# Performance work log

Measured on AMD Instinct MI355X. Metric: run time of the kernel, lower is better.

Reference implementation:

```python
import jax, jax.numpy as jnp
import numpy as np

B, L, F = 16, 1080, 2
D = 128          # d_model
NC = 64          # num_cnn_channels
DIN = 256        # expand * d_model
N = 16           # d_state
K = 4            # d_conv
R = 8            # dt_rank = ceil(d_model/16)
OUT = 3
NB = 3           # num_mamba_blocks


def setup_inputs() -> dict:
    key = jax.random.key(0)
    ks = jax.random.split(key, 24)
    nrm = lambda k, shape, s=0.05: (jax.random.normal(k, shape) * s).astype(jnp.float32)
    bn = lambda c: jnp.stack([jnp.ones(c), jnp.zeros(c), jnp.zeros(c), jnp.ones(c)]).astype(jnp.float32)
    return {
        'x': jax.random.normal(ks[0], (B, L, F), dtype=jnp.float32),
        'emb_W': nrm(ks[1], (F, D), 0.5), 'emb_b': jnp.zeros(D, jnp.float32),
        'c3_W': nrm(ks[2], (NC, D, 3)), 'c3_b': jnp.zeros(NC, jnp.float32), 'bn3': bn(NC),
        'c5_W': nrm(ks[3], (NC, D, 5)), 'c5_b': jnp.zeros(NC, jnp.float32), 'bn5': bn(NC),
        'c7_W': nrm(ks[4], (NC, D, 7)), 'c7_b': jnp.zeros(NC, jnp.float32), 'bn7': bn(NC),
        'cf_W': nrm(ks[5], (D, 3 * NC, 1)), 'cf_b': jnp.zeros(D, jnp.float32), 'bnf': bn(D),
        'ln_g': jnp.ones((NB, D), jnp.float32), 'ln_b': jnp.zeros((NB, D), jnp.float32),
        'in_W': nrm(ks[6], (NB, 2 * DIN, D)),
        'mconv_W': nrm(ks[7], (NB, DIN, K), 0.2), 'mconv_b': jnp.zeros((NB, DIN), jnp.float32),
        'xproj_W': nrm(ks[8], (NB, R + 2 * N, DIN)),
        'dt_W': nrm(ks[9], (NB, DIN, R), 0.1), 'dt_b': jnp.full((NB, DIN), -1.0, jnp.float32),
        'A_log': jnp.tile(jnp.log(jnp.arange(1.0, N + 1.0, dtype=jnp.float32)), (NB, DIN, 1)),
        'Dp': jnp.ones((NB, DIN), jnp.float32),
        'out_W': nrm(ks[10], (NB, D, DIN)),
        'flin_W': nrm(ks[11], (D, 2 * D)), 'flin_b': jnp.zeros(D, jnp.float32),
        'fc_W': nrm(ks[12], (OUT, D)), 'fc_b': jnp.zeros(OUT, jnp.float32),
    }


def conv1d(x, W, b, pad):
    # x: (B,C,L), W: (O,C,K)
    y = jax.lax.conv_general_dilated(x, W, (1,), [(pad, pad)],
                                     dimension_numbers=('NCH', 'OIH', 'NCH'))
    return y + b[None, :, None]


def bn_relu(x, bn, eps=1e-5):
    g, b, m, v = bn  # each (C,)
    return jax.nn.relu((x - m[None, :, None]) * (g / jnp.sqrt(v + eps))[None, :, None] + b[None, :, None])


def layernorm(x, g, b, eps=1e-5):
    mu = x.mean(-1, keepdims=True)
    var = ((x - mu) ** 2).mean(-1, keepdims=True)
    return (x - mu) / jnp.sqrt(var + eps) * g + b


def pos_encoding(seq_len, d_model):
    pos = jnp.arange(seq_len, dtype=jnp.float32)[:, None]
    div = jnp.exp(jnp.arange(0, d_model, 2, dtype=jnp.float32) * (-np.log(10000.0) / d_model))
    pe = jnp.zeros((seq_len, d_model), jnp.float32)
    pe = pe.at[:, 0::2].set(jnp.sin(pos * div)).at[:, 1::2].set(jnp.cos(pos * div))
    return pe


def selective_scan(u, dt, A, Bm, Cm, Dp):
    # u,dt: (b,l,d); A: (d,n); Bm,Cm: (b,l,n); Dp: (d,)
    dA = jnp.exp(dt[..., None] * A)                    # (b,l,d,n)
    dBu = (dt * u)[..., None] * Bm[:, :, None, :]      # (b,l,d,n)

    def step(h, t):
        dA_t, dBu_t, C_t = t
        h = dA_t * h + dBu_t                           # (b,d,n)
        return h, jnp.einsum('bdn,bn->bd', h, C_t)

    h0 = jnp.zeros((u.shape[0], u.shape[2], A.shape[1]), u.dtype)
    _, ys = jax.lax.scan(step, h0, (jnp.swapaxes(dA, 0, 1), jnp.swapaxes(dBu, 0, 1), jnp.swapaxes(Cm, 0, 1)))
    return jnp.swapaxes(ys, 0, 1) + u * Dp


def mamba_block(x, in_W, conv_W, conv_b, xproj_W, dt_W, dt_b, A_log, Dp, out_W):
    xz = x @ in_W.T                                    # (b,l,2*din)
    xs, z = jnp.split(xz, 2, axis=-1)
    xc = jnp.swapaxes(xs, 1, 2)                        # (b,din,l)
    xc = jax.lax.conv_general_dilated(xc, conv_W[:, None, :], (1,), [(K - 1, 0)],
                                      dimension_numbers=('NCH', 'OIH', 'NCH'),
                                      feature_group_count=DIN)
    u = jax.nn.silu(jnp.swapaxes(xc + conv_b[None, :, None], 1, 2))  # (b,l,din)
    dbl = u @ xproj_W.T
    dt, Bm, Cm = dbl[..., :R], dbl[..., R:R + N], dbl[..., R + N:]
    dt = jax.nn.softplus(dt @ dt_W.T + dt_b)
    A = -jnp.exp(A_log)
    y = selective_scan(u, dt, A, Bm, Cm, Dp)
    return (y * jax.nn.silu(z)) @ out_W.T


def reference(x, emb_W, emb_b, c3_W, c3_b, bn3, c5_W, c5_b, bn5, c7_W, c7_b, bn7,
              cf_W, cf_b, bnf, ln_g, ln_b, in_W, mconv_W, mconv_b, xproj_W,
              dt_W, dt_b, A_log, Dp, out_W, flin_W, flin_b, fc_W, fc_b):
    xe = x @ emb_W + emb_b + pos_encoding(x.shape[1], emb_W.shape[1])  # (B,L,D)
    ci = jnp.swapaxes(xe, 1, 2)                                        # (B,D,L)
    o3 = bn_relu(conv1d(ci, c3_W, c3_b, 1), bn3)
    o5 = bn_relu(conv1d(ci, c5_W, c5_b, 2), bn5)
    o7 = bn_relu(conv1d(ci, c7_W, c7_b, 3), bn7)
    cc = jnp.concatenate([o3, o5, o7], axis=1)                         # (B,3*NC,L)
    cf = bn_relu(conv1d(cc, cf_W, cf_b, 0), bnf)
    cnn_feat = jnp.swapaxes(cf, 1, 2)                                  # (B,L,D)
    m = xe
    for i in range(NB):  # Sequential(LN, Mamba, Dropout) -- no residual, dropout=eval
        m = mamba_block(layernorm(m, ln_g[i], ln_b[i]), in_W[i], mconv_W[i], mconv_b[i],
                        xproj_W[i], dt_W[i], dt_b[i], A_log[i], Dp[i], out_W[i])
    fused = jax.nn.relu(jnp.concatenate([cnn_feat, m], axis=-1) @ flin_W.T + flin_b)
    pooled = fused.mean(axis=1)                                        # AdaptiveAvgPool1d(1)
    return pooled @ fc_W.T + fc_b
```

## Files before the change

### kernel.cpp

```cpp
#include <hip/hip_runtime.h>
#include <math.h>

#define LSEQ   1080
#define NBATCH 16
#define BLROWS (LSEQ*NBATCH)
#define CHN    27
#define LCH    40

typedef __bf16  bf16x8 __attribute__((ext_vector_type(8)));
typedef float   f32x4  __attribute__((ext_vector_type(4)));
typedef short   short8 __attribute__((ext_vector_type(8)));
typedef short   short4v __attribute__((ext_vector_type(4)));

__device__ __forceinline__ float silu_f(float x) { return x / (1.f + __expf(-x)); }

__device__ __forceinline__ unsigned short f2bf(float f) {
    unsigned int u = __float_as_uint(f);
    u += 0x7fffu + ((u >> 16) & 1u);
    return (unsigned short)(u >> 16);
}
__device__ __forceinline__ float bf2f(unsigned short h) {
    return __uint_as_float(((unsigned int)h) << 16);
}
__device__ __forceinline__ void split_bf(float v, unsigned short& h, unsigned short& l) {
    h = f2bf(v);
    l = f2bf(v - bf2f(h));
}

__global__ __launch_bounds__(256) void embed_kernel(
    const float* __restrict__ x, const float* __restrict__ embW,
    const float* __restrict__ embb, float* __restrict__ xe,
    unsigned short* __restrict__ xeh, unsigned short* __restrict__ xel)
{
    int idx = blockIdx.x * 256 + threadIdx.x;
    if (idx >= BLROWS * 128) return;
    int d = idx & 127;
    int r = idx >> 7;
    int t = r % LSEQ;
    float x0 = x[(size_t)r * 2], x1 = x[(size_t)r * 2 + 1];
    int i2 = d & 126;
    float div = expf((float)i2 * (-9.210340371976184f / 128.f));
    float arg = (float)t * div;
    float pe = (d & 1) ? cosf(arg) : sinf(arg);
    float v = fmaf(x0, embW[d], fmaf(x1, embW[128 + d], embb[d] + pe));
    xe[idx] = v;
    unsigned short h, l;
    split_bf(v, h, l);
    xeh[idx] = h; xel[idx] = l;
}

#define JOB_W192  172032
#define JOB_CF    196608
#define JOB_IN    393216
#define JOB_XP    442368
#define JOB_OT    540672
#define JOB_FL    573440
#define JOB_END   574080
__global__ __launch_bounds__(256) void convw_all(
    const float* __restrict__ c3W, const float* __restrict__ c5W,
    const float* __restrict__ c7W, const float* __restrict__ cfW,
    const float* __restrict__ inW, const float* __restrict__ xpW,
    const float* __restrict__ otW, const float* __restrict__ flW,
    const float* __restrict__ c3b, const float* __restrict__ c5b, const float* __restrict__ c7b,
    const float* __restrict__ bn3, const float* __restrict__ bn5, const float* __restrict__ bn7,
    const float* __restrict__ cfb, const float* __restrict__ bnf,
    unsigned short* __restrict__ w192h, unsigned short* __restrict__ w192l,
    unsigned short* __restrict__ cfh, unsigned short* __restrict__ cfl,
    unsigned short* __restrict__ inh, unsigned short* __restrict__ inl,
    unsigned short* __restrict__ xph, unsigned short* __restrict__ xpl,
    unsigned short* __restrict__ oth, unsigned short* __restrict__ otl,
    unsigned short* __restrict__ flh, unsigned short* __restrict__ fll,
    float* __restrict__ schpack)
{
    int idx = blockIdx.x * 256 + threadIdx.x;
    if (idx >= JOB_END) return;
    float v;
    unsigned short *dh, *dl;
    int off;
    if (idx < JOB_W192) {
        off = idx;
        int n = off / 896, kk = off % 896;
        int slot = kk >> 7, d = kk & 127;
        int br = n >> 6, c = n & 63;
        int KT = 3 + 2 * br, pad = 1 + br;
        int tp = slot - 3 + pad;
        const float* w = (br == 0) ? c3W : (br == 1) ? c5W : c7W;
        v = (tp >= 0 && tp < KT) ? w[((c << 7) + d) * KT + tp] : 0.f;
        dh = w192h; dl = w192l;
    } else if (idx < JOB_CF) {
        off = idx - JOB_W192; v = cfW[off]; dh = cfh; dl = cfl;
    } else if (idx < JOB_IN) {
        off = idx - JOB_CF; v = inW[off]; dh = inh; dl = inl;
    } else if (idx < JOB_XP) {
        off = idx - JOB_IN;
        int k = off & 255, n = (off >> 8) & 63, blk = off >> 14;
        v = (n < 40) ? xpW[((size_t)blk * 40 + n) * 256 + k] : 0.f;
        dh = xph; dl = xpl;
    } else if (idx < JOB_OT) {
        off = idx - JOB_XP; v = otW[off]; dh = oth; dl = otl;
    } else if (idx < JOB_FL) {
        off = idx - JOB_OT; v = flW[off]; dh = flh; dl = fll;
    } else {
        int j = idx - JOB_FL;
        if (j < 384) {
            int col = (j < 192) ? j : j - 192;
            int isSh = j >= 192;
            int br = col >> 6, c = col & 63;
            const float* bn = (br == 0) ? bn3 : (br == 1) ? bn5 : bn7;
            float bias = ((br == 0) ? c3b : (br == 1) ? c5b : c7b)[c];
            float g = bn[c], bb = bn[64 + c], m = bn[128 + c], vv = bn[192 + c];
            float scale = g * rsqrtf(vv + 1e-5f);
            float shift = (bias - m) * scale + bb;
            schpack[j] = isSh ? shift : scale;
        } else {
            int j2 = j - 384;
            int col = j2 & 127;
            int isSh = j2 >= 128;
            float g = bnf[col], bb = bnf[128 + col], m = bnf[256 + col], vv = bnf[384 + col];
            float scale = g * rsqrtf(vv + 1e-5f);
            float shift = (cfb[col] - m) * scale + bb;
            schpack[384 + j2] = isSh ? shift : scale;
        }
        return;
    }
    unsigned short h, l;
    split_bf(v, h, l);
    dh[off] = h; dl[off] = l;
}

__global__ __launch_bounds__(256) void gemm_conv(
    const unsigned short* __restrict__ Xh, const unsigned short* __restrict__ Xl,
    const unsigned short* __restrict__ Wh, const unsigned short* __restrict__ Wl,
    const float* __restrict__ sc, const float* __restrict__ sh,
    unsigned short* __restrict__ Ch, unsigned short* __restrict__ Cl)
{
    __shared__ unsigned short Ah[70][40], Al[70][40];
    __shared__ unsigned short Bh[64][136], Bl[64][136];
    const int tid = threadIdx.x;
    const int n0 = blockIdx.x * 64, t0 = blockIdx.y * 64, b = blockIdx.z;
    const size_t boff = (size_t)b * LSEQ;
    const int lane = tid & 63, wid = tid >> 6;
    const int wr = wid >> 1, wc = wid & 1;
    const int fr = lane & 15, fq = lane >> 4;
    const short8 zz = {0, 0, 0, 0, 0, 0, 0, 0};
    f32x4 acc[2][2];
#pragma unroll
    for (int m = 0; m < 2; ++m)
#pragma unroll
        for (int n = 0; n < 2; ++n) acc[m][n] = (f32x4){0.f, 0.f, 0.f, 0.f};

    for (int ks = 0; ks < 128; ks += 32) {
#pragma unroll
        for (int l = 0; l < 2; ++l) {
            int c = tid + l * 256;
            if (c < 280) {
                int row = c >> 2, kc = (c & 3) << 3;
                int ts = t0 - 3 + row;
                short8 vh = zz, vl = zz;
                if (ts >= 0 && ts < LSEQ) {
                    size_t s = (boff + ts) * 128 + ks + kc;
                    vh = *(const short8*)&Xh[s];
                    vl = *(const short8*)&Xl[s];
                }
                *(short8*)&Ah[row][kc] = vh;
                *(short8*)&Al[row][kc] = vl;
            }
        }
        for (int g = 0; g < 2; ++g) {
            const int ntap = (g == 0) ? 4 : 3;
#pragma unroll
            for (int l = 0; l < 4; ++l) {
                int c = tid + l * 256;
                int col = c >> 4, rem = c & 15, tt = rem >> 2, kq = (rem & 3) << 3;
                if (tt < ntap) {
                    int tap = g * 4 + tt;
                    size_t s = (size_t)(n0 + col) * 896 + tap * 128 + ks + kq;
                    *(short8*)&Bh[col][tt * 32 + kq] = *(const short8*)&Wh[s];
                    *(short8*)&Bl[col][tt * 32 + kq] = *(const short8*)&Wl[s];
                }
            }
            __syncthreads();
            for (int tt = 0; tt < ntap; ++tt) {
                int tap = g * 4 + tt;
                bf16x8 bhf[2], blf[2];
#pragma unroll
                for (int n = 0; n < 2; ++n) {
                    int col = wc * 32 + n * 16 + fr;
                    bhf[n] = __builtin_bit_cast(bf16x8, *(const short8*)&Bh[col][tt * 32 + fq * 8]);
                    blf[n] = __builtin_bit_cast(bf16x8, *(const short8*)&Bl[col][tt * 32 + fq * 8]);
                }
#pragma unroll
                for (int m = 0; m < 2; ++m) {
                    int rowA = wr * 32 + m * 16 + fr + tap;
                    bf16x8 ahf = __builtin_bit_cast(bf16x8, *(const short8*)&Ah[rowA][fq * 8]);
                    bf16x8 alf = __builtin_bit_cast(bf16x8, *(const short8*)&Al[rowA][fq * 8]);
#pragma unroll
                    for (int n = 0; n < 2; ++n) {
                        acc[m][n] = __builtin_amdgcn_mfma_f32_16x16x32_bf16(ahf, bhf[n], acc[m][n], 0, 0, 0);
                        acc[m][n] = __builtin_amdgcn_mfma_f32_16x16x32_bf16(ahf, blf[n], acc[m][n], 0, 0, 0);
                        acc[m][n] = __builtin_amdgcn_mfma_f32_16x16x32_bf16(alf, bhf[n], acc[m][n], 0, 0, 0);
                    }
                }
            }
            __syncthreads();
        }
    }
    unsigned short* Chb = Ch + (size_t)b * LSEQ * 192;
    unsigned short* Clb = Cl + (size_t)b * LSEQ * 192;
#pragma unroll
    for (int m = 0; m < 2; ++m) {
#pragma unroll
        for (int n = 0; n < 2; ++n) {
            int colg = n0 + wc * 32 + n * 16 + fr;
            float scl = sc[colg], shf2 = sh[colg];
#pragma unroll
            for (int r = 0; r < 4; ++r) {
                int t = t0 + wr * 32 + m * 16 + fq * 4 + r;
                if (t >= LSEQ) continue;
                float v = fmaf(acc[m][n][r], scl, shf2);
                v = v > 0.f ? v : 0.f;
                unsigned short h, l;
                split_bf(v, h, l);
                Chb[(size_t)t * 192 + colg] = h;
                Clb[(size_t)t * 192 + colg] = l;
            }
        }
    }
}

template<int BM, int BN>
__global__ __launch_bounds__(256) void gemm_plain(
    const unsigned short* __restrict__ Aph, const unsigned short* __restrict__ Apl, int lda,
    const unsigned short* __restrict__ Wh, const unsigned short* __restrict__ Wl, int Kd,
    int Ntot, int epi,
    const float* __restrict__ sc, const float* __restrict__ sh, const float* __restrict__ bias,
    float* __restrict__ Cf, int ldc,
    unsigned short* __restrict__ Ch, unsigned short* __restrict__ Cl, int ldch)
{
    constexpr int WM = BM / 2, WN = BN / 2;
    constexpr int MR = WM / 16, NR = WN / 16;
    constexpr int ACH = (BM * 4) / 256;
    constexpr int BCH = (BN * 4) / 256;
    __shared__ unsigned short Ah[BM][40], Al[BM][40];
    __shared__ unsigned short Bh[BN][40], Bl[BN][40];
    const int tid = threadIdx.x;
    const int b = blockIdx.z, t0 = blockIdx.y * BM, n0 = blockIdx.x * BN;
    const unsigned short* Abh = Aph + (size_t)b * LSEQ * lda;
    const unsigned short* Abl = Apl + (size_t)b * LSEQ * lda;
    const int lane = tid & 63, wid = tid >> 6;
    const int wr = wid >> 1, wc = wid & 1;
    const int fr = lane & 15, fq = lane >> 4;
    f32x4 acc[MR][NR];
#pragma unroll
    for (int m = 0; m < MR; ++m)
#pragma unroll
        for (int n = 0; n < NR; ++n) acc[m][n] = (f32x4){0.f, 0.f, 0.f, 0.f};

    const short8 zz = {0, 0, 0, 0, 0, 0, 0, 0};
    for (int ks = 0; ks < Kd; ks += 32) {
#pragma unroll
        for (int l = 0; l < ACH; ++l) {
            int c = tid + l * 256;
            int row = c >> 2, kc = (c & 3) << 3;
            int t = t0 + row;
            short8 vh = zz, vl = zz;
            if (t < LSEQ) {
                size_t s = (size_t)t * lda + ks + kc;
                vh = *(const short8*)&Abh[s];
                vl = *(const short8*)&Abl[s];
            }
            *(short8*)&Ah[row][kc] = vh;
            *(short8*)&Al[row][kc] = vl;
        }
#pragma unroll
        for (int l = 0; l < BCH; ++l) {
            int c = tid + l * 256;
            int col = c >> 2, kc = (c & 3) << 3;
            size_t s = (size_t)(n0 + col) * Kd + ks + kc;
            *(short8*)&Bh[col][kc] = *(const short8*)&Wh[s];
            *(short8*)&Bl[col][kc] = *(const short8*)&Wl[s];
        }
        __syncthreads();
        bf16x8 bhf[NR], blf[NR];
#pragma unroll
        for (int n = 0; n < NR; ++n) {
            int col = wc * WN + n * 16 + fr;
            bhf[n] = __builtin_bit_cast(bf16x8, *(const short8*)&Bh[col][fq * 8]);
            blf[n] = __builtin_bit_cast(bf16x8, *(const short8*)&Bl[col][fq * 8]);
        }
#pragma unroll
        for (int m = 0; m < MR; ++m) {
            int rowr = wr * WM + m * 16 + fr;
            bf16x8 ahf = __builtin_bit_cast(bf16x8, *(const short8*)&Ah[rowr][fq * 8]);
            bf16x8 alf = __builtin_bit_cast(bf16x8, *(const short8*)&Al[rowr][fq * 8]);
#pragma unroll
            for (int n = 0; n < NR; ++n) {
                acc[m][n] = __builtin_amdgcn_mfma_f32_16x16x32_bf16(ahf, bhf[n], acc[m][n], 0, 0, 0);
                acc[m][n] = __builtin_amdgcn_mfma_f32_16x16x32_bf16(ahf, blf[n], acc[m][n], 0, 0, 0);
                acc[m][n] = __builtin_amdgcn_mfma_f32_16x16x32_bf16(alf, bhf[n], acc[m][n], 0, 0, 0);
            }
        }
        __syncthreads();
    }

    float* Cfb = Cf ? Cf + (size_t)b * LSEQ * ldc : nullptr;
    unsigned short* Chb = Ch ? Ch + (size_t)b * LSEQ * ldch : nullptr;
    unsigned short* Clb = Cl ? Cl + (size_t)b * LSEQ * ldch : nullptr;
#pragma unroll
    for (int m = 0; m < MR; ++m) {
#pragma unroll
        for (int n = 0; n < NR; ++n) {
            int colg = n0 + wc * WN + n * 16 + fr;
            if (colg >= Ntot) continue;
#pragma unroll
            for (int r = 0; r < 4; ++r) {
                int t = t0 + wr * WM + m * 16 + fq * 4 + r;
                if (t >= LSEQ) continue;
                float v = acc[m][n][r];
                if (epi == 0) {
                    Cfb[(size_t)t * ldc + colg] = v;
                } else if (epi == 1) {
                    v = fmaf(v, sc[colg], sh[colg]);
                    v = v > 0.f ? v : 0.f;
                    unsigned short h, l;
                    split_bf(v, h, l);
                    Chb[(size_t)t * ldch + colg] = h;
                    Clb[(size_t)t * ldch + colg] = l;
                } else if (epi == 2) {
                    v += bias[colg];
                    v = v > 0.f ? v : 0.f;
                    Cfb[(size_t)t * ldc + colg] = v;
                } else {
                    unsigned short h, l;
                    split_bf(v, h, l);
                    Chb[(size_t)t * ldch + colg] = h;
                    Clb[(size_t)t * ldch + colg] = l;
                }
            }
        }
    }
}

__global__ __launch_bounds__(256) void ln_kernel(
    const float* __restrict__ in, const float* __restrict__ g,
    const float* __restrict__ b2, unsigned short* __restrict__ oh,
    unsigned short* __restrict__ ol)
{
    int lane = threadIdx.x & 63;
    int wid  = threadIdx.x >> 6;
    int row = blockIdx.x * 4 + wid;
    if (row >= BLROWS) return;
    const float* rp = in + (size_t)row * 128;
    float v0 = rp[lane], v1 = rp[lane + 64];
    float s = v0 + v1;
#pragma unroll
    for (int o2 = 32; o2 > 0; o2 >>= 1) s += __shfl_xor(s, o2, 64);
    float mu = s * (1.f / 128.f);
    float d0 = v0 - mu, d1 = v1 - mu;
    float q = d0 * d0 + d1 * d1;
#pragma unroll
    for (int o2 = 32; o2 > 0; o2 >>= 1) q += __shfl_xor(q, o2, 64);
    float rs = 1.f / sqrtf(q * (1.f / 128.f) + 1e-5f);
    float y0 = d0 * rs * g[lane]      + b2[lane];
    float y1 = d1 * rs * g[lane + 64] + b2[lane + 64];
    unsigned short h, l;
    size_t o = (size_t)row * 128;
    split_bf(y0, h, l); oh[o + lane] = h;      ol[o + lane] = l;
    split_bf(y1, h, l); oh[o + lane + 64] = h; ol[o + lane + 64] = l;
}

__global__ __launch_bounds__(256) void mconv_kernel(
    const float* __restrict__ xz, const float* __restrict__ Wc,
    const float* __restrict__ bc, float* __restrict__ u,
    unsigned short* __restrict__ uh, unsigned short* __restrict__ ul)
{
    int idx = blockIdx.x * 256 + threadIdx.x;
    int c = idx & 255;
    int r = idx >> 8;
    if (r >= BLROWS) return;
    int t = r % LSEQ;
    const float* xs = xz + (size_t)r * 512 + c;
    float acc = bc[c];
    if (t >= 3) acc = fmaf(xs[-3 * 512], Wc[c * 4 + 0], acc);
    if (t >= 2) acc = fmaf(xs[-2 * 512], Wc[c * 4 + 1], acc);
    if (t >= 1) acc = fmaf(xs[-1 * 512], Wc[c * 4 + 2], acc);
    acc = fmaf(xs[0], Wc[c * 4 + 3], acc);
    float uv = silu_f(acc);
    size_t o = (size_t)r * 256 + c;
    u[o] = uv;
    unsigned short h, l;
    split_bf(uv, h, l);
    uh[o] = h; ul[o] = l;
}

__global__ __launch_bounds__(256) void dtk_kernel(
    const float* __restrict__ dbl, const float* __restrict__ dtW,
    const float* __restrict__ dtb, float* __restrict__ dtout)
{
    int idx = blockIdx.x * 256 + threadIdx.x;
    int c = idx & 255;
    int r = idx >> 8;
    if (r >= BLROWS) return;
    const float* dr = dbl + (size_t)r * 40;
    float a = dtb[c];
#pragma unroll
    for (int j = 0; j < 8; ++j) a = fmaf(dr[j], dtW[c * 8 + j], a);
    float sp = (a > 20.f) ? a : log1pf(__expf(a));
    dtout[(size_t)r * 256 + c] = sp;
}

__global__ __launch_bounds__(256) void scan1_kernel(
    const float* __restrict__ dt, const float* __restrict__ u,
    const float* __restrict__ dbl, const float* __restrict__ Alog,
    float* __restrict__ P, float* __restrict__ S)
{
    __shared__ float sdt[40][64], su[40][64], sB[40][16];
    int bid = blockIdx.x;
    int dg = bid & 3;
    int rest = bid >> 2;
    int ch = rest % CHN;
    int b  = rest / CHN;
    int tid = threadIdx.x;
    int ng = tid & 3, di = tid >> 2;
    int d0 = dg * 64, d = d0 + di, n0 = ng * 4;
    int r0 = b * LSEQ + ch * LCH;
#pragma unroll
    for (int l = 0; l < 3; ++l) {
        int j = tid + l * 256;
        if (j < 640) {
            int row = j >> 4, q = (j & 15) << 2;
            size_t s = (size_t)(r0 + row) * 256 + d0 + q;
            *(float4*)&sdt[row][q] = *(const float4*)&dt[s];
            *(float4*)&su [row][q] = *(const float4*)&u [s];
        }
    }
    if (tid < 160) {
        int row = tid >> 2, q = (tid & 3) << 2;
        *(float4*)&sB[row][q] = *(const float4*)&dbl[(size_t)(r0 + row) * 40 + 8 + q];
    }
    float A2[4];
#pragma unroll
    for (int j = 0; j < 4; ++j) A2[j] = -__expf(Alog[d * 16 + n0 + j]);
    float p[4] = {1.f, 1.f, 1.f, 1.f}, s[4] = {0.f, 0.f, 0.f, 0.f};
    __syncthreads();
#pragma unroll 4
    for (int qi = 0; qi < LCH; ++qi) {
        float dtv = sdt[qi][di];
        float dtu = dtv * su[qi][di];
        float4 Br = *(const float4*)&sB[qi][n0];
        float bv[4] = {Br.x, Br.y, Br.z, Br.w};
#pragma unroll
        for (int j = 0; j < 4; ++j) {
            float a = __expf(dtv * A2[j]);
            p[j] *= a;
            s[j] = fmaf(a, s[j], dtu * bv[j]);
        }
    }
    size_t ob = ((size_t)(b * CHN + ch) * 256 + d) * 16 + n0;
    *(float4*)&P[ob] = make_float4(p[0], p[1], p[2], p[3]);
    *(float4*)&S[ob] = make_float4(s[0], s[1], s[2], s[3]);
}

__global__ __launch_bounds__(256) void scan2_kernel(
    const float* __restrict__ P, const float* __restrict__ S, float* __restrict__ H0)
{
    int idx = blockIdx.x * 256 + threadIdx.x;
    int n = idx & 15;
    int d = (idx >> 4) & 255;
    int b = idx >> 12;
    float h = 0.f;
    for (int ch = 0; ch < CHN; ++ch) {
        size_t o = ((size_t)(b * CHN + ch) * 256 + d) * 16 + n;
        H0[o] = h;
        h = fmaf(P[o], h, S[o]);
    }
}

__global__ __launch_bounds__(256) void scan3_kernel(
    const float* __restrict__ dt, const float* __restrict__ u,
    const float* __restrict__ dbl, const float* __restrict__ Alog,
    const float* __restrict__ H0, const float* __restrict__ Dp,
    const float* __restrict__ xz, unsigned short* __restrict__ gh,
    unsigned short* __restrict__ gl)
{
    __shared__ float sdt[40][64], su[40][64], sz[40][64], sB[40][16], sC[40][16];
    int bid = blockIdx.x;
    int dg = bid & 3;
    int rest = bid >> 2;
    int ch = rest % CHN;
    int b  = rest / CHN;
    int tid = threadIdx.x;
    int ng = tid & 3, di = tid >> 2;
    int d0 = dg * 64, d = d0 + di, n0 = ng * 4;
    int r0 = b * LSEQ + ch * LCH;
#pragma unroll
    for (int l = 0; l < 3; ++l) {
        int j = tid + l * 256;
        if (j < 640) {
            int row = j >> 4, q = (j & 15) << 2;
            size_t s = (size_t)(r0 + row) * 256 + d0 + q;
            *(float4*)&sdt[row][q] = *(const float4*)&dt[s];
            *(float4*)&su [row][q] = *(const float4*)&u [s];
            *(float4*)&sz [row][q] = *(const float4*)&xz[(size_t)(r0 + row) * 512 + 256 + d0 + q];
        }
    }
    if (tid < 160) {
        int row = tid >> 2, q = (tid & 3) << 2;
        *(float4*)&sB[row][q] = *(const float4*)&dbl[(size_t)(r0 + row) * 40 + 8 + q];
        *(float4*)&sC[row][q] = *(const float4*)&dbl[(size_t)(r0 + row) * 40 + 24 + q];
    }
    float A2[4];
#pragma unroll
    for (int j = 0; j < 4; ++j) A2[j] = -__expf(Alog[d * 16 + n0 + j]);
    size_t ob = ((size_t)(b * CHN + ch) * 256 + d) * 16 + n0;
    float4 h4 = *(const float4*)&H0[ob];
    float h[4] = {h4.x, h4.y, h4.z, h4.w};
    float Dpd = Dp[d];
    __syncthreads();
    for (int qi = 0; qi < LCH; ++qi) {
        float dtv = sdt[qi][di];
        float uv  = su[qi][di];
        float dtu = dtv * uv;
        float4 Br = *(const float4*)&sB[qi][n0];
        float4 Cr = *(const float4*)&sC[qi][n0];
        float bv[4] = {Br.x, Br.y, Br.z, Br.w};
        float cv[4] = {Cr.x, Cr.y, Cr.z, Cr.w};
        float pacc = 0.f;
#pragma unroll
        for (int j = 0; j < 4; ++j) {
            float a = __expf(dtv * A2[j]);
            h[j] = fmaf(a, h[j], dtu * bv[j]);
            pacc = fmaf(h[j], cv[j], pacc);
        }
        float acc = pacc + __shfl_xor(pacc, 1);
        acc += __shfl_xor(acc, 2);
        float yv = fmaf(uv, Dpd, acc);
        float gv = yv * silu_f(sz[qi][di]);
        if (ng == 0) sz[qi][di] = gv;
    }
    __syncthreads();
#pragma unroll
    for (int l = 0; l < 3; ++l) {
        int j = tid + l * 256;
        if (j < 640) {
            int row = j >> 4, q = (j & 15) << 2;
            float4 gv4 = *(const float4*)&sz[row][q];
            float gv[4] = {gv4.x, gv4.y, gv4.z, gv4.w};
            alignas(8) unsigned short hs[4], ls[4];
#pragma unroll
            for (int jj = 0; jj < 4; ++jj) split_bf(gv[jj], hs[jj], ls[jj]);
            size_t o = (size_t)(r0 + row) * 256 + d0 + q;
            *(short4v*)&gh[o] = *(short4v*)hs;
            *(short4v*)&gl[o] = *(short4v*)ls;
        }
    }
}

__global__ __launch_bounds__(128) void pool1_kernel(
    const float* __restrict__ fused, float* __restrict__ part)
{
    int d = threadIdx.x;
    int blk = blockIdx.x;
    int ch = blk % CHN;
    int b  = blk / CHN;
    int t0 = ch * LCH;
    float s = 0.f;
    for (int q = 0; q < LCH; ++q)
        s += fused[((size_t)(b * LSEQ + t0 + q)) * 128 + d];
    part[(size_t)(b * CHN + ch) * 128 + d] = s;
}

__global__ __launch_bounds__(128) void pool2_kernel(
    const float* __restrict__ part, const float* __restrict__ fcW,
    const float* __restrict__ fcb, float* __restrict__ out)
{
    __shared__ float pl[128];
    int d = threadIdx.x;
    int b = blockIdx.x;
    float s = 0.f;
    for (int ch = 0; ch < CHN; ++ch) s += part[(size_t)(b * CHN + ch) * 128 + d];
    pl[d] = s * (1.f / 1080.f);
    __syncthreads();
    if (d < 3) {
        float a = fcb[d];
        for (int dd = 0; dd < 128; ++dd) a = fmaf(pl[dd], fcW[d * 128 + dd], a);
        out[b * 3 + d] = a;
    }
}

extern "C" void kernel_launch(void* const* d_in, const int* in_sizes, int n_in,
                              void* d_out, int out_size, void* d_ws, size_t ws_size,
                              hipStream_t stream)
{
    const float* x    = (const float*)d_in[0];
    const float* embW = (const float*)d_in[1];
    const float* embb = (const float*)d_in[2];
    const float* c3W  = (const float*)d_in[3];
    const float* c3b  = (const float*)d_in[4];
    const float* bn3  = (const float*)d_in[5];
    const float* c5W  = (const float*)d_in[6];
    const float* c5b  = (const float*)d_in[7];
    const float* bn5  = (const float*)d_in[8];
    const float* c7W  = (const float*)d_in[9];
    const float* c7b  = (const float*)d_in[10];
    const float* bn7  = (const float*)d_in[11];
    const float* cfW  = (const float*)d_in[12];
    const float* cfb  = (const float*)d_in[13];
    const float* bnf  = (const float*)d_in[14];
    const float* lng  = (const float*)d_in[15];
    const float* lnb  = (const float*)d_in[16];
    const float* inW  = (const float*)d_in[17];
    const float* mcW  = (const float*)d_in[18];
    const float* mcb  = (const float*)d_in[19];
    const float* xpW  = (const float*)d_in[20];
    const float* dtW  = (const float*)d_in[21];
    const float* dtbp = (const float*)d_in[22];
    const float* Alog = (const float*)d_in[23];
    const float* Dp   = (const float*)d_in[24];
    const float* outW = (const float*)d_in[25];
    const float* flW  = (const float*)d_in[26];
    const float* flb  = (const float*)d_in[27];
    const float* fcW  = (const float*)d_in[28];
    const float* fcb  = (const float*)d_in[29];

    float* ws = (float*)d_ws;
    size_t off = 0;
    auto alloc = [&](size_t n) { float* p = ws + off; off += n; return p; };
    float* xe   = alloc((size_t)BLROWS * 128);
    float* xz   = alloc((size_t)BLROWS * 512);
    float* ub   = alloc((size_t)BLROWS * 256);
    float* dtt  = alloc((size_t)BLROWS * 256);
    float* dbl  = alloc((size_t)BLROWS * 40);
    float* Pb   = alloc((size_t)NBATCH * CHN * 256 * 16);
    float* Sb   = alloc((size_t)NBATCH * CHN * 256 * 16);
    float* h0b  = alloc((size_t)NBATCH * CHN * 256 * 16);
    float* schpack = alloc(640);
    float* fused = xz;
    float* mtail = xz + (size_t)BLROWS * 384;

    off = (off + 3) & ~(size_t)3;
    unsigned short* us = (unsigned short*)(ws + off);
    size_t uo = 0;
    auto ualloc = [&](size_t n) { unsigned short* p = us + uo; uo += n; return p; };
    unsigned short* cch  = ualloc((size_t)BLROWS * 192);
    unsigned short* ccl  = ualloc((size_t)BLROWS * 192);
    unsigned short* finh = ualloc((size_t)BLROWS * 256);
    unsigned short* finl = ualloc((size_t)BLROWS * 256);
    unsigned short* ubh  = ualloc((size_t)BLROWS * 256);
    unsigned short* ubl  = ualloc((size_t)BLROWS * 256);
    unsigned short* xeh  = ualloc((size_t)BLROWS * 128);
    unsigned short* xel  = ualloc((size_t)BLROWS * 128);
    unsigned short* w192h = ualloc((size_t)192 * 896); unsigned short* w192l = ualloc((size_t)192 * 896);
    unsigned short* cfh = ualloc(128 * 192); unsigned short* cfl = ualloc(128 * 192);
    unsigned short* inh = ualloc((size_t)1536 * 128); unsigned short* inl = ualloc((size_t)1536 * 128);
    unsigned short* xph = ualloc((size_t)3 * 64 * 256); unsigned short* xpl = ualloc((size_t)3 * 64 * 256);
    unsigned short* oth = ualloc((size_t)384 * 256); unsigned short* otl = ualloc((size_t)384 * 256);
    unsigned short* flh = ualloc((size_t)128 * 256); unsigned short* fll = ualloc((size_t)128 * 256);
    unsigned short* lnxh = cch;
    unsigned short* lnxl = ccl;
    unsigned short* gbh  = ubh;
    unsigned short* gbl  = ubl;
    (void)ws_size; (void)in_sizes; (void)n_in; (void)out_size;

    convw_all<<<(JOB_END + 255) / 256, 256, 0, stream>>>(
        c3W, c5W, c7W, cfW, inW, xpW, outW, flW,
        c3b, c5b, c7b, bn3, bn5, bn7, cfb, bnf,
        w192h, w192l, cfh, cfl, inh, inl, xph, xpl, oth, otl, flh, fll, schpack);

    embed_kernel<<<(BLROWS * 128) / 256, 256, 0, stream>>>(x, embW, embb, xe, xeh, xel);

    dim3 gconv(3, 17, NBATCH);
    gemm_conv<<<gconv, 256, 0, stream>>>(xeh, xel, w192h, w192l, schpack, schpack + 192, cch, ccl);
    dim3 g17(1, 17, NBATCH);
    gemm_plain<64, 128><<<g17, 256, 0, stream>>>(
        cch, ccl, 192, cfh, cfl, 192, 128, 1,
        schpack + 384, schpack + 512, nullptr, nullptr, 0, finh, finl, 256);

    const int SCAN_BLKS = NBATCH * CHN * 4;
    for (int i = 0; i < 3; ++i) {
        const float* min_ = (i == 0) ? xe : mtail;

        ln_kernel<<<BLROWS / 4, 256, 0, stream>>>(min_, lng + i * 128, lnb + i * 128, lnxh, lnxl);

        dim3 gin(4, 17, NBATCH);
        gemm_plain<64, 128><<<gin, 256, 0, stream>>>(
            lnxh, lnxl, 128, inh + (size_t)i * 512 * 128, inl + (size_t)i * 512 * 128, 128,
            512, 0, nullptr, nullptr, nullptr, xz, 512, nullptr, nullptr, 0);

        mconv_kernel<<<BLROWS, 256, 0, stream>>>(xz, mcW + i * 256 * 4, mcb + i * 256, ub, ubh, ubl);

        gemm_plain<64, 64><<<g17, 256, 0, stream>>>(
            ubh, ubl, 256, xph + (size_t)i * 64 * 256, xpl + (size_t)i * 64 * 256, 256,
            40, 0, nullptr, nullptr, nullptr, dbl, 40, nullptr, nullptr, 0);

        dtk_kernel<<<BLROWS, 256, 0, stream>>>(dbl, dtW + i * 256 * 8, dtbp + i * 256, dtt);

        scan1_kernel<<<SCAN_BLKS, 256, 0, stream>>>(
            dtt, ub, dbl, Alog + i * 256 * 16, Pb, Sb);
        scan2_kernel<<<(NBATCH * 256 * 16) / 256, 256, 0, stream>>>(Pb, Sb, h0b);
        scan3_kernel<<<SCAN_BLKS, 256, 0, stream>>>(
            dtt, ub, dbl, Alog + i * 256 * 16, h0b, Dp + i * 256, xz, gbh, gbl);

        if (i < 2) {
            gemm_plain<64, 128><<<g17, 256, 0, stream>>>(
                gbh, gbl, 256, oth + (size_t)i * 128 * 256, otl + (size_t)i * 128 * 256, 256,
                128, 0, nullptr, nullptr, nullptr, mtail, 128, nullptr, nullptr, 0);
        } else {
            gemm_plain<64, 128><<<g17, 256, 0, stream>>>(
                gbh, gbl, 256, oth + (size_t)i * 128 * 256, otl + (size_t)i * 128 * 256, 256,
                128, 3, nullptr, nullptr, nullptr, nullptr, 0, finh + 128, finl + 128, 256);
        }
    }

    gemm_plain<64, 128><<<g17, 256, 0, stream>>>(
        finh, finl, 256, flh, fll, 256, 128, 2,
        nullptr, nullptr, flb, fused, 128, nullptr, nullptr, 0);

    pool1_kernel<<<NBATCH * CHN, 128, 0, stream>>>(fused, Pb);
    pool2_kernel<<<NBATCH, 128, 0, stream>>>(Pb, fcW, fcb, (float*)d_out);
}
```

Before: 648.6 us.

## Fold dt projection into x_proj GEMM and fuse LayerNorm into out-proj epilogue

Precomputes a combined weight, dtW·xpW_dt, so that a single GEMM produces both the dt pre-activation (with bias and softplus applied in the epilogue) and the B/C columns. This removes the separate dtk kernel and the intermediate dbl round trip. The out-projection GEMM for blocks 0 and 1 now computes a LayerNorm over the 128 output columns in its epilogue and writes bf16 hi/lo directly, which drops two ln_kernel launches and the fp32 mtail buffer. The trade-offs are a wider x_proj GEMM (288 columns instead of 40) and an extra cross-warp reduction with syncs in the out-proj epilogue.

```diff
diff --git a/kernel.cpp b/kernel.cpp
--- a/kernel.cpp
+++ b/kernel.cpp
@@ -52,22 +52,23 @@
 #define JOB_W192  172032
 #define JOB_CF    196608
 #define JOB_IN    393216
-#define JOB_XP    442368
-#define JOB_OT    540672
-#define JOB_FL    573440
-#define JOB_END   574080
+#define JOB_WX    638976
+#define JOB_OT    737280
+#define JOB_FL    770048
+#define JOB_END   770688
 __global__ __launch_bounds__(256) void convw_all(
     const float* __restrict__ c3W, const float* __restrict__ c5W,
     const float* __restrict__ c7W, const float* __restrict__ cfW,
     const float* __restrict__ inW, const float* __restrict__ xpW,
-    const float* __restrict__ otW, const float* __restrict__ flW,
+    const float* __restrict__ dtW, const float* __restrict__ otW,
+    const float* __restrict__ flW,
     const float* __restrict__ c3b, const float* __restrict__ c5b, const float* __restrict__ c7b,
     const float* __restrict__ bn3, const float* __restrict__ bn5, const float* __restrict__ bn7,
     const float* __restrict__ cfb, const float* __restrict__ bnf,
     unsigned short* __restrict__ w192h, unsigned short* __restrict__ w192l,
     unsigned short* __restrict__ cfh, unsigned short* __restrict__ cfl,
     unsigned short* __restrict__ inh, unsigned short* __restrict__ inl,
-    unsigned short* __restrict__ xph, unsigned short* __restrict__ xpl,
+    unsigned short* __restrict__ wxh, unsigned short* __restrict__ wxl,
     unsigned short* __restrict__ oth, unsigned short* __restrict__ otl,
     unsigned short* __restrict__ flh, unsigned short* __restrict__ fll,
     float* __restrict__ schpack)
@@ -91,13 +92,26 @@
         off = idx - JOB_W192; v = cfW[off]; dh = cfh; dl = cfl;
     } else if (idx < JOB_IN) {
         off = idx - JOB_CF; v = inW[off]; dh = inh; dl = inl;
-    } else if (idx < JOB_XP) {
+    } else if (idx < JOB_WX) {
         off = idx - JOB_IN;
-        int k = off & 255, n = (off >> 8) & 63, blk = off >> 14;
-        v = (n < 40) ? xpW[((size_t)blk * 40 + n) * 256 + k] : 0.f;
-        dh = xph; dl = xpl;
+        int k = off & 255;
+        int row = (off >> 8) % 320;
+        int blk = off / 81920;
+        if (row < 256) {
+            const float* dw = dtW + (size_t)blk * 2048 + row * 8;
+            const float* xp = xpW + (size_t)blk * 10240 + k;
+            float a = 0.f;
+#pragma unroll
+            for (int j = 0; j < 8; ++j) a = fmaf(dw[j], xp[j * 256], a);
+            v = a;
+        } else if (row < 288) {
+            v = xpW[(size_t)blk * 10240 + (row - 256 + 8) * 256 + k];
+        } else {
+            v = 0.f;
+        }
+        dh = wxh; dl = wxl;
     } else if (idx < JOB_OT) {
-        off = idx - JOB_XP; v = otW[off]; dh = oth; dl = otl;
+        off = idx - JOB_WX; v = otW[off]; dh = oth; dl = otl;
     } else if (idx < JOB_FL) {
         off = idx - JOB_OT; v = flW[off]; dh = flh; dl = fll;
     } else {
@@ -235,7 +249,8 @@
     int Ntot, int epi,
     const float* __restrict__ sc, const float* __restrict__ sh, const float* __restrict__ bias,
     float* __restrict__ Cf, int ldc,
-    unsigned short* __restrict__ Ch, unsigned short* __restrict__ Cl, int ldch)
+    unsigned short* __restrict__ Ch, unsigned short* __restrict__ Cl, int ldch,
+    float* __restrict__ Cf2, int ldc2)
 {
     constexpr int WM = BM / 2, WN = BN / 2;
     constexpr int MR = WM / 16, NR = WN / 16;
@@ -304,8 +319,90 @@
     }
 
     float* Cfb = Cf ? Cf + (size_t)b * LSEQ * ldc : nullptr;
+    float* Cf2b = Cf2 ? Cf2 + (size_t)b * LSEQ * ldc2 : nullptr;
     unsigned short* Chb = Ch ? Ch + (size_t)b * LSEQ * ldch : nullptr;
     unsigned short* Clb = Cl ? Cl + (size_t)b * LSEQ * ldch : nullptr;
+
+    if (epi == 4) {
+        float* red = reinterpret_cast<float*>(&Ah[0][0]);
+        float part[MR][4], mu[MR][4], rs[MR][4];
+#pragma unroll
+        for (int m = 0; m < MR; ++m)
+#pragma unroll
+            for (int r = 0; r < 4; ++r) {
+                float p = 0.f;
+#pragma unroll
+                for (int n = 0; n < NR; ++n) p += acc[m][n][r];
+#pragma unroll
+                for (int o2 = 1; o2 < 16; o2 <<= 1) p += __shfl_xor(p, o2, 64);
+                part[m][r] = p;
+            }
+        if (fr == 0) {
+#pragma unroll
+            for (int m = 0; m < MR; ++m)
+#pragma unroll
+                for (int r = 0; r < 4; ++r)
+                    red[(wr * 32 + m * 16 + fq * 4 + r) * 2 + wc] = part[m][r];
+        }
+        __syncthreads();
+#pragma unroll
+        for (int m = 0; m < MR; ++m)
+#pragma unroll
+            for (int r = 0; r < 4; ++r) {
+                int row = wr * 32 + m * 16 + fq * 4 + r;
+                mu[m][r] = (red[row * 2] + red[row * 2 + 1]) * (1.f / 128.f);
+            }
+        __syncthreads();
+#pragma unroll
+        for (int m = 0; m < MR; ++m)
+#pragma unroll
+            for (int r = 0; r < 4; ++r) {
+                float p = 0.f;
+#pragma unroll
+                for (int n = 0; n < NR; ++n) {
+                    float dv = acc[m][n][r] - mu[m][r];
+                    p = fmaf(dv, dv, p);
+                }
+#pragma unroll
+                for (int o2 = 1; o2 < 16; o2 <<= 1) p += __shfl_xor(p, o2, 64);
+                part[m][r] = p;
+            }
+        if (fr == 0) {
+#pragma unroll
+            for (int m = 0; m < MR; ++m)
+#pragma unroll
+                for (int r = 0; r < 4; ++r)
+                    red[(wr * 32 + m * 16 + fq * 4 + r) * 2 + wc] = part[m][r];
+        }
+        __syncthreads();
+#pragma unroll
+        for (int m = 0; m < MR; ++m)
+#pragma unroll
+            for (int r = 0; r < 4; ++r) {
+                int row = wr * 32 + m * 16 + fq * 4 + r;
+                rs[m][r] = rsqrtf((red[row * 2] + red[row * 2 + 1]) * (1.f / 128.f) + 1e-5f);
+            }
+#pragma unroll
+        for (int m = 0; m < MR; ++m) {
+#pragma unroll
+            for (int n = 0; n < NR; ++n) {
+                int colg = wc * WN + n * 16 + fr;
+                float g = sc[colg], b2 = sh[colg];
+#pragma unroll
+                for (int r = 0; r < 4; ++r) {
+                    int t = t0 + wr * WM + m * 16 + fq * 4 + r;
+                    if (t >= LSEQ) continue;
+                    float v = (acc[m][n][r] - mu[m][r]) * rs[m][r] * g + b2;
+                    unsigned short h, l;
+                    split_bf(v, h, l);
+                    Chb[(size_t)t * ldch + colg] = h;
+                    Clb[(size_t)t * ldch + colg] = l;
+                }
+            }
+        }
+        return;
+    }
+
 #pragma unroll
     for (int m = 0; m < MR; ++m) {
 #pragma unroll
@@ -330,11 +427,19 @@
                     v += bias[colg];
                     v = v > 0.f ? v : 0.f;
                     Cfb[(size_t)t * ldc + colg] = v;
-                } else {
+                } else if (epi == 3) {
                     unsigned short h, l;
                     split_bf(v, h, l);
                     Chb[(size_t)t * ldch + colg] = h;
                     Clb[(size_t)t * ldch + colg] = l;
+                } else {
+                    if (colg < 256) {
+                        float v2 = v + bias[colg];
+                        float sp = (v2 > 20.f) ? v2 : log1pf(__expf(v2));
+                        Cfb[(size_t)t * ldc + colg] = sp;
+                    } else {
+                        Cf2b[(size_t)t * ldc2 + (colg - 256)] = v;
+                    }
                 }
             }
         }
@@ -393,25 +498,9 @@
     uh[o] = h; ul[o] = l;
 }
 
-__global__ __launch_bounds__(256) void dtk_kernel(
-    const float* __restrict__ dbl, const float* __restrict__ dtW,
-    const float* __restrict__ dtb, float* __restrict__ dtout)
-{
-    int idx = blockIdx.x * 256 + threadIdx.x;
-    int c = idx & 255;
-    int r = idx >> 8;
-    if (r >= BLROWS) return;
-    const float* dr = dbl + (size_t)r * 40;
-    float a = dtb[c];
-#pragma unroll
-    for (int j = 0; j < 8; ++j) a = fmaf(dr[j], dtW[c * 8 + j], a);
-    float sp = (a > 20.f) ? a : log1pf(__expf(a));
-    dtout[(size_t)r * 256 + c] = sp;
-}
-
 __global__ __launch_bounds__(256) void scan1_kernel(
     const float* __restrict__ dt, const float* __restrict__ u,
-    const float* __restrict__ dbl, const float* __restrict__ Alog,
+    const float* __restrict__ dbl32, const float* __restrict__ Alog,
     float* __restrict__ P, float* __restrict__ S)
 {
     __shared__ float sdt[40][64], su[40][64], sB[40][16];
@@ -436,7 +525,7 @@
     }
     if (tid < 160) {
         int row = tid >> 2, q = (tid & 3) << 2;
-        *(float4*)&sB[row][q] = *(const float4*)&dbl[(size_t)(r0 + row) * 40 + 8 + q];
+        *(float4*)&sB[row][q] = *(const float4*)&dbl32[(size_t)(r0 + row) * 32 + q];
     }
     float A2[4];
 #pragma unroll
@@ -478,7 +567,7 @@
 
 __global__ __launch_bounds__(256) void scan3_kernel(
     const float* __restrict__ dt, const float* __restrict__ u,
-    const float* __restrict__ dbl, const float* __restrict__ Alog,
+    const float* __restrict__ dbl32, const float* __restrict__ Alog,
     const float* __restrict__ H0, const float* __restrict__ Dp,
     const float* __restrict__ xz, unsigned short* __restrict__ gh,
     unsigned short* __restrict__ gl)
@@ -506,8 +595,8 @@
     }
     if (tid < 160) {
         int row = tid >> 2, q = (tid & 3) << 2;
-        *(float4*)&sB[row][q] = *(const float4*)&dbl[(size_t)(r0 + row) * 40 + 8 + q];
-        *(float4*)&sC[row][q] = *(const float4*)&dbl[(size_t)(r0 + row) * 40 + 24 + q];
+        *(float4*)&sB[row][q] = *(const float4*)&dbl32[(size_t)(r0 + row) * 32 + q];
+        *(float4*)&sC[row][q] = *(const float4*)&dbl32[(size_t)(r0 + row) * 32 + 16 + q];
     }
     float A2[4];
 #pragma unroll
@@ -626,17 +715,16 @@
     float* ws = (float*)d_ws;
     size_t off = 0;
     auto alloc = [&](size_t n) { float* p = ws + off; off += n; return p; };
-    float* xe   = alloc((size_t)BLROWS * 128);
-    float* xz   = alloc((size_t)BLROWS * 512);
-    float* ub   = alloc((size_t)BLROWS * 256);
-    float* dtt  = alloc((size_t)BLROWS * 256);
-    float* dbl  = alloc((size_t)BLROWS * 40);
-    float* Pb   = alloc((size_t)NBATCH * CHN * 256 * 16);
-    float* Sb   = alloc((size_t)NBATCH * CHN * 256 * 16);
-    float* h0b  = alloc((size_t)NBATCH * CHN * 256 * 16);
+    float* xe    = alloc((size_t)BLROWS * 128);
+    float* xz    = alloc((size_t)BLROWS * 512);
+    float* ub    = alloc((size_t)BLROWS * 256);
+    float* dtt   = alloc((size_t)BLROWS * 256);
+    float* dbl32 = alloc((size_t)BLROWS * 32);
+    float* Pb    = alloc((size_t)NBATCH * CHN * 256 * 16);
+    float* Sb    = alloc((size_t)NBATCH * CHN * 256 * 16);
+    float* h0b   = alloc((size_t)NBATCH * CHN * 256 * 16);
     float* schpack = alloc(640);
     float* fused = xz;
-    float* mtail = xz + (size_t)BLROWS * 384;
 
     off = (off + 3) & ~(size_t)3;
     unsigned short* us = (unsigned short*)(ws + off);
@@ -653,7 +741,7 @@
     unsigned short* w192h = ualloc((size_t)192 * 896); unsigned short* w192l = ualloc((size_t)192 * 896);
     unsigned short* cfh = ualloc(128 * 192); unsigned short* cfl = ualloc(128 * 192);
     unsigned short* inh = ualloc((size_t)1536 * 128); unsigned short* inl = ualloc((size_t)1536 * 128);
-    unsigned short* xph = ualloc((size_t)3 * 64 * 256); unsigned short* xpl = ualloc((size_t)3 * 64 * 256);
+    unsigned short* wxh = ualloc((size_t)3 * 320 * 256); unsigned short* wxl = ualloc((size_t)3 * 320 * 256);
     unsigned short* oth = ualloc((size_t)384 * 256); unsigned short* otl = ualloc((size_t)384 * 256);
     unsigned short* flh = ualloc((size_t)128 * 256); unsigned short* fll = ualloc((size_t)128 * 256);
     unsigned short* lnxh = cch;
@@ -663,9 +751,9 @@
     (void)ws_size; (void)in_sizes; (void)n_in; (void)out_size;
 
     convw_all<<<(JOB_END + 255) / 256, 256, 0, stream>>>(
-        c3W, c5W, c7W, cfW, inW, xpW, outW, flW,
+        c3W, c5W, c7W, cfW, inW, xpW, dtW, outW, flW,
         c3b, c5b, c7b, bn3, bn5, bn7, cfb, bnf,
-        w192h, w192l, cfh, cfl, inh, inl, xph, xpl, oth, otl, flh, fll, schpack);
+        w192h, w192l, cfh, cfl, inh, inl, wxh, wxl, oth, otl, flh, fll, schpack);
 
     embed_kernel<<<(BLROWS * 128) / 256, 256, 0, stream>>>(x, embW, embb, xe, xeh, xel);
 
@@ -674,47 +762,45 @@
     dim3 g17(1, 17, NBATCH);
     gemm_plain<64, 128><<<g17, 256, 0, stream>>>(
         cch, ccl, 192, cfh, cfl, 192, 128, 1,
-        schpack + 384, schpack + 512, nullptr, nullptr, 0, finh, finl, 256);
+        schpack + 384, schpack + 512, nullptr, nullptr, 0, finh, finl, 256, nullptr, 0);
+
+    ln_kernel<<<BLROWS / 4, 256, 0, stream>>>(xe, lng, lnb, lnxh, lnxl);
 
     const int SCAN_BLKS = NBATCH * CHN * 4;
     for (int i = 0; i < 3; ++i) {
-        const float* min_ = (i == 0) ? xe : mtail;
-
-        ln_kernel<<<BLROWS / 4, 256, 0, stream>>>(min_, lng + i * 128, lnb + i * 128, lnxh, lnxl);
-
         dim3 gin(4, 17, NBATCH);
         gemm_plain<64, 128><<<gin, 256, 0, stream>>>(
             lnxh, lnxl, 128, inh + (size_t)i * 512 * 128, inl + (size_t)i * 512 * 128, 128,
-            512, 0, nullptr, nullptr, nullptr, xz, 512, nullptr, nullptr, 0);
+            512, 0, nullptr, nullptr, nullptr, xz, 512, nullptr, nullptr, 0, nullptr, 0);
 
         mconv_kernel<<<BLROWS, 256, 0, stream>>>(xz, mcW + i * 256 * 4, mcb + i * 256, ub, ubh, ubl);
 
-        gemm_plain<64, 64><<<g17, 256, 0, stream>>>(
-            ubh, ubl, 256, xph + (size_t)i * 64 * 256, xpl + (size_t)i * 64 * 256, 256,
-            40, 0, nullptr, nullptr, nullptr, dbl, 40, nullptr, nullptr, 0);
-
-        dtk_kernel<<<BLROWS, 256, 0, stream>>>(dbl, dtW + i * 256 * 8, dtbp + i * 256, dtt);
+        dim3 gxp(5, 17, NBATCH);
+        gemm_plain<64, 64><<<gxp, 256, 0, stream>>>(
+            ubh, ubl, 256, wxh + (size_t)i * 320 * 256, wxl + (size_t)i * 320 * 256, 256,
+            288, 5, nullptr, nullptr, dtbp + i * 256, dtt, 256, nullptr, nullptr, 0, dbl32, 32);
 
         scan1_kernel<<<SCAN_BLKS, 256, 0, stream>>>(
-            dtt, ub, dbl, Alog + i * 256 * 16, Pb, Sb);
+            dtt, ub, dbl32, Alog + i * 256 * 16, Pb, Sb);
         scan2_kernel<<<(NBATCH * 256 * 16) / 256, 256, 0, stream>>>(Pb, Sb, h0b);
         scan3_kernel<<<SCAN_BLKS, 256, 0, stream>>>(
-            dtt, ub, dbl, Alog + i * 256 * 16, h0b, Dp + i * 256, xz, gbh, gbl);
+            dtt, ub, dbl32, Alog + i * 256 * 16, h0b, Dp + i * 256, xz, gbh, gbl);
 
         if (i < 2) {
             gemm_plain<64, 128><<<g17, 256, 0, stream>>>(
                 gbh, gbl, 256, oth + (size_t)i * 128 * 256, otl + (size_t)i * 128 * 256, 256,
-                128, 0, nullptr, nullptr, nullptr, mtail, 128, nullptr, nullptr, 0);
+                128, 4, lng + (i + 1) * 128, lnb + (i + 1) * 128, nullptr,
+                nullptr, 0, lnxh, lnxl, 128, nullptr, 0);
         } else {
             gemm_plain<64, 128><<<g17, 256, 0, stream>>>(
                 gbh, gbl, 256, oth + (size_t)i * 128 * 256, otl + (size_t)i * 128 * 256, 256,
-                128, 3, nullptr, nullptr, nullptr, nullptr, 0, finh + 128, finl + 128, 256);
+                128, 3, nullptr, nullptr, nullptr, nullptr, 0, finh + 128, finl + 128, 256, nullptr, 0);
         }
     }
 
     gemm_plain<64, 128><<<g17, 256, 0, stream>>>(
         finh, finl, 256, flh, fll, 256, 128, 2,
-        nullptr, nullptr, flb, fused, 128, nullptr, nullptr, 0);
+        nullptr, nullptr, flb, fused, 128, nullptr, nullptr, 0, nullptr, 0);
 
     pool1_kernel<<<NBATCH * CHN, 128, 0, stream>>>(fused, Pb);
     pool2_kernel<<<NBATCH, 128, 0, stream>>>(Pb, fcW, fcb, (float*)d_out);
```

After: 689.8 us. 6.4% more time.
